# Kernel optimization log

Hardware: AMD Instinct MI355X
Metric: run time of the kernel (lower is better)

## Reference

```python
import jax, jax.numpy as jnp
import numpy as np

B, T, C = 2, 4096, 768
H = 12
HD = C // H  # 64


def setup_inputs() -> dict:
    key = jax.random.key(0)
    k1, k2, k3 = jax.random.split(key, 3)
    scale = 0.02
    x = jax.random.normal(k1, (B, T, C), dtype=jnp.float32)
    w_attn = jax.random.normal(k2, (C, 3 * C), dtype=jnp.float32) * scale
    b_attn = jnp.zeros((3 * C,), dtype=jnp.float32)
    w_proj = jax.random.normal(k3, (C, C), dtype=jnp.float32) * scale
    b_proj = jnp.zeros((C,), dtype=jnp.float32)
    return {"x": x, "w_attn": w_attn, "b_attn": b_attn,
            "w_proj": w_proj, "b_proj": b_proj}


def reference(x, w_attn, b_attn, w_proj, b_proj):
    b, t, c = x.shape
    # QKV projection: (B,T,3C)
    qkv = x @ w_attn + b_attn
    q, k, v = jnp.split(qkv, 3, axis=2)
    # (B,H,T,HD)
    q = q.reshape(b, t, H, HD).transpose(0, 2, 1, 3)
    k = k.reshape(b, t, H, HD).transpose(0, 2, 1, 3)
    v = v.reshape(b, t, H, HD).transpose(0, 2, 1, 3)
    # scores: (B,H,T,T)
    scores = jnp.einsum('bhqd,bhkd->bhqk', q, k) / jnp.sqrt(jnp.float32(HD))
    causal = jnp.tril(jnp.ones((t, t), dtype=bool))
    scores = jnp.where(causal[None, None, :, :], scores, -jnp.inf)
    att = jax.nn.softmax(scores, axis=-1)
    # attn_dropout p=0 -> identity
    y = jnp.einsum('bhqk,bhkd->bhqd', att, v)
    y = y.transpose(0, 2, 1, 3).reshape(b, t, c)
    # output projection (resid_dropout p=0 -> identity)
    return y @ w_proj + b_proj
```

## Files before the change

### kernel.cpp

```cpp
#include <hip/hip_runtime.h>


typedef unsigned short u16;
typedef unsigned int u32;
using bf16x8 = __attribute__((ext_vector_type(8))) short;
using f32x4  = __attribute__((ext_vector_type(4))) float;

__device__ __forceinline__ float bf2f(u16 u) {
  return __uint_as_float(((u32)u) << 16);
}
__device__ __forceinline__ u16 f2bf(float f) {
  u32 u = __float_as_uint(f);
  u += 0x7fffu + ((u >> 16) & 1u);
  return (u16)(u >> 16);
}
__device__ __forceinline__ u32 cvtpk(float lo, float hi) {
  u32 r;
  asm("v_cvt_pk_bf16_f32 %0, %1, %2" : "=v"(r) : "v"(lo), "v"(hi));
  return r;
}

__global__ void fill_sentinel_f32(float* __restrict__ out, int n, float v) {
  const int i0 = blockIdx.x * blockDim.x + threadIdx.x;
  const int stride = gridDim.x * blockDim.x;
  for (int i = i0; i < n; i += stride) out[i] = v;
}

__global__ void convert_f32_bf16(const float* __restrict__ src, u16* __restrict__ dst,
                                 int n) {
  const int i0 = blockIdx.x * blockDim.x + threadIdx.x;
  const int stride = gridDim.x * blockDim.x;
  for (int i = i0; i < n; i += stride) dst[i] = f2bf(src[i]);
}

__global__ void transpose_f32_bf16(const float* __restrict__ in, u16* __restrict__ out,
                                   int R, int C) {
  __shared__ u16 tile[32][33];
  const int c0 = blockIdx.x * 32, r0 = blockIdx.y * 32;
  const int tx = threadIdx.x & 31, ty = threadIdx.x >> 5;
#pragma unroll
  for (int i = 0; i < 32; i += 8)
    tile[ty + i][tx] = f2bf(in[(size_t)(r0 + ty + i) * C + c0 + tx]);
  __syncthreads();
#pragma unroll
  for (int i = 0; i < 32; i += 8)
    out[(size_t)(c0 + ty + i) * R + r0 + tx] = tile[tx][ty + i];
}

#define LDT 72
#define QSCALE 0.18033688011112f

__device__ __forceinline__ void stage_tile(u16* lds, const u16* g, int ld, int tid) {
#pragma unroll
  for (int i = 0; i < 4; ++i) {
    const int idx = i * 256 + tid;
    const int r = idx >> 3, c = (idx & 7) * 8;
    *(uint4*)&lds[r * LDT + c] = *(const uint4*)&g[(size_t)r * ld + c];
  }
}

template <int MODE>
__global__ __launch_bounds__(256, 2)
void gemm128(const u16* __restrict__ A, const u16* __restrict__ Bt,
             const u16* __restrict__ bias, void* __restrict__ O0v,
             u16* __restrict__ O1, u16* __restrict__ O2, int Kd) {
  __shared__ __align__(16) u16 As[128 * LDT];
  __shared__ __align__(16) u16 Bs[128 * LDT];
  const int tid = threadIdx.x;
  const int lane = tid & 63, wave = tid >> 6;
  const int wm = wave >> 1, wn = wave & 1;
  const int l16 = lane & 15, quad = lane >> 4;

  const u16* Ag = A + (size_t)blockIdx.x * 128 * Kd;
  const u16* Bg = Bt + (size_t)blockIdx.y * 128 * Kd;

  f32x4 acc[4][4] = {};
  for (int kt = 0; kt < Kd; kt += 64) {
    stage_tile(As, Ag + kt, Kd, tid);
    stage_tile(Bs, Bg + kt, Kd, tid);
    __syncthreads();
#pragma unroll
    for (int s = 0; s < 2; ++s) {
      bf16x8 af[4], bfr[4];
#pragma unroll
      for (int i = 0; i < 4; ++i) {
        const int m = wm * 64 + i * 16 + l16;
        af[i] = *(const bf16x8*)&As[m * LDT + (s * 4 + quad) * 8];
        const int n = wn * 64 + i * 16 + l16;
        bfr[i] = *(const bf16x8*)&Bs[n * LDT + (s * 4 + quad) * 8];
      }
#pragma unroll
      for (int i = 0; i < 4; ++i)
#pragma unroll
        for (int j = 0; j < 4; ++j)
          acc[i][j] = __builtin_amdgcn_mfma_f32_16x16x32_bf16(af[i], bfr[j],
                                                              acc[i][j], 0, 0, 0);
    }
    __syncthreads();
  }

#pragma unroll
  for (int i = 0; i < 4; ++i) {
    const int mbase = blockIdx.x * 128 + wm * 64 + i * 16 + quad * 4;
#pragma unroll
    for (int j = 0; j < 4; ++j) {
      const int n = blockIdx.y * 128 + wn * 64 + j * 16 + l16;
      const float bv = bf2f(bias[n]);
#pragma unroll
      for (int r = 0; r < 4; ++r) {
        const int m = mbase + r;
        float ov = acc[i][j][r] + bv;
        if (MODE == 0) {
          const int b = m >> 12, t = m & 4095;
          const int which = n / 768;
          const int c = n - which * 768;
          const int h = c >> 6, d = c & 63;
          const size_t bh = (size_t)b * 12 + h;
          if (which == 0) {
            ((u16*)O0v)[((bh * 4096 + t) << 6) + d] = f2bf(ov * QSCALE);
          } else if (which == 1) {
            O1[((bh * 4096 + t) << 6) + d] = f2bf(ov);
          } else {
            O2[((bh << 6) + d) * 4096 + t] = f2bf(ov);
          }
        } else {
          ((float*)O0v)[(size_t)m * 768 + n] = ov;
        }
      }
    }
  }
}

__global__ __launch_bounds__(256, 4)
void attn_chunk(const u16* __restrict__ Q, const u16* __restrict__ K,
                const u16* __restrict__ Vt, u16* __restrict__ Y,
                u16* __restrict__ part_o, float* __restrict__ part_l) {
  const int idx = blockIdx.x;
  const int bh = idx % 24;
  const int cid = 79 - (idx / 24);
  int qt = 0, base = 0, nc = 1;
  for (int q = 0; q < 32; ++q) {
    const int c = (q >> 3) + 1;
    if (cid < base + c) { qt = q; nc = c; break; }
    base += c;
  }
  const int j = cid - base;
  const int Nt = 2 * qt + 2;
  const int kbeg = j * 16;
  const int kend = (kbeg + 16 < Nt) ? kbeg + 16 : Nt;
  const int q0 = qt * 128;
  const int b = bh / 12, h = bh % 12;
  const size_t ho = (size_t)bh * 4096 * 64;
  const u16* Qg = Q + ho + (size_t)q0 * 64;
  const u16* Kg = K + ho;
  const u16* Vg = Vt + ho;

  __shared__ __align__(16) u16 Ks[64 * LDT];
  __shared__ __align__(16) u16 Vs[64 * LDT];

  const int tid = threadIdx.x;
  const int lane = tid & 63, wave = tid >> 6;
  const int l16 = lane & 15, quad = lane >> 4;

  bf16x8 qf[2][2];
#pragma unroll
  for (int rt = 0; rt < 2; ++rt)
#pragma unroll
    for (int s = 0; s < 2; ++s)
      qf[rt][s] = *(const bf16x8*)&Qg[(wave * 32 + rt * 16 + l16) * 64 + s * 32 + quad * 8];

  float lsum[2] = {};
  f32x4 o[2][4] = {};

  for (int kt2 = kbeg; kt2 < kend; ++kt2) {
    const int t0 = kt2 * 64;
    __syncthreads();
    {
      int c = tid;
      *(uint4*)&Ks[(c >> 3) * LDT + (c & 7) * 8] =
          *(const uint4*)&Kg[(size_t)(t0 + (c >> 3)) * 64 + (c & 7) * 8];
      c = tid + 256;
      *(uint4*)&Ks[(c >> 3) * LDT + (c & 7) * 8] =
          *(const uint4*)&Kg[(size_t)(t0 + (c >> 3)) * 64 + (c & 7) * 8];
      c = tid;
      *(uint4*)&Vs[(c >> 3) * LDT + (c & 7) * 8] =
          *(const uint4*)&Vg[(size_t)(c >> 3) * 4096 + t0 + (c & 7) * 8];
      c = tid + 256;
      *(uint4*)&Vs[(c >> 3) * LDT + (c & 7) * 8] =
          *(const uint4*)&Vg[(size_t)(c >> 3) * 4096 + t0 + (c & 7) * 8];
    }
    __syncthreads();

    f32x4 sc[4][2] = {};
#pragma unroll
    for (int s = 0; s < 2; ++s) {
      bf16x8 kf[4];
#pragma unroll
      for (int nt = 0; nt < 4; ++nt)
        kf[nt] = *(const bf16x8*)&Ks[(nt * 16 + l16) * LDT + s * 32 + quad * 8];
#pragma unroll
      for (int nt = 0; nt < 4; ++nt)
#pragma unroll
        for (int rt = 0; rt < 2; ++rt)
          sc[nt][rt] = __builtin_amdgcn_mfma_f32_16x16x32_bf16(kf[nt], qf[rt][s],
                                                               sc[nt][rt], 0, 0, 0);
    }

    u32 pw[4][2][2];
#pragma unroll
    for (int rt = 0; rt < 2; ++rt) {
      const int rowb = q0 + wave * 32 + rt * 16;
      if (t0 + 63 <= rowb) {
#pragma unroll
        for (int nt = 0; nt < 4; ++nt) {
          f32x4 p;
#pragma unroll
          for (int r = 0; r < 4; ++r) {
            p[r] = __builtin_amdgcn_exp2f(sc[nt][rt][r]);
            lsum[rt] += p[r];
          }
          pw[nt][rt][0] = cvtpk(p[0], p[1]);
          pw[nt][rt][1] = cvtpk(p[2], p[3]);
        }
      } else {
        const int qrow = rowb + l16;
#pragma unroll
        for (int nt = 0; nt < 4; ++nt) {
          f32x4 p;
#pragma unroll
          for (int r = 0; r < 4; ++r) {
            float pv = __builtin_amdgcn_exp2f(sc[nt][rt][r]);
            if (t0 + nt * 16 + quad * 4 + r > qrow) pv = 0.f;
            p[r] = pv;
            lsum[rt] += pv;
          }
          pw[nt][rt][0] = cvtpk(p[0], p[1]);
          pw[nt][rt][1] = cvtpk(p[2], p[3]);
        }
      }
    }

#pragma unroll
    for (int s2 = 0; s2 < 2; ++s2) {
      bf16x8 vf[4];
#pragma unroll
      for (int dt = 0; dt < 4; ++dt) {
        const u16* vp = &Vs[(dt * 16 + l16) * LDT + s2 * 32 + quad * 4];
        union { uint2 h[2]; bf16x8 v; } uv;
        uv.h[0] = *(const uint2*)vp;
        uv.h[1] = *(const uint2*)(vp + 16);
        vf[dt] = uv.v;
      }
#pragma unroll
      for (int rt = 0; rt < 2; ++rt) {
        union { u32 w[4]; bf16x8 v; } up;
        up.w[0] = pw[2 * s2][rt][0];
        up.w[1] = pw[2 * s2][rt][1];
        up.w[2] = pw[2 * s2 + 1][rt][0];
        up.w[3] = pw[2 * s2 + 1][rt][1];
#pragma unroll
        for (int dt = 0; dt < 4; ++dt)
          o[rt][dt] = __builtin_amdgcn_mfma_f32_16x16x32_bf16(up.v, vf[dt],
                                                              o[rt][dt], 0, 0, 0);
      }
    }
  }

  float red[2];
#pragma unroll
  for (int rt = 0; rt < 2; ++rt) {
    float rs = lsum[rt];
    rs += __shfl_xor(rs, 16);
    rs += __shfl_xor(rs, 32);
    red[rt] = rs;
  }

  if (nc == 1) {
#pragma unroll
    for (int rt = 0; rt < 2; ++rt)
#pragma unroll
      for (int r = 0; r < 4; ++r) {
        const float inv = 1.f / __shfl(red[rt], quad * 4 + r);
        const int t = q0 + wave * 32 + rt * 16 + quad * 4 + r;
#pragma unroll
        for (int dt = 0; dt < 4; ++dt)
          Y[((size_t)b * 4096 + t) * 768 + h * 64 + dt * 16 + l16] =
              f2bf(o[rt][dt][r] * inv);
      }
  } else {
    const int pslot = bh * 72 + (cid - 8);
    u16* po = part_o + (size_t)pslot * 8192;
    float* pl = part_l + pslot * 128;
#pragma unroll
    for (int rt = 0; rt < 2; ++rt)
#pragma unroll
      for (int r = 0; r < 4; ++r) {
        const float rs = __shfl(red[rt], quad * 4 + r);
        const int row = wave * 32 + rt * 16 + quad * 4 + r;
#pragma unroll
        for (int dt = 0; dt < 4; ++dt)
          po[row * 64 + dt * 16 + l16] = f2bf(o[rt][dt][r]);
        if (l16 == 0) pl[row] = rs;
      }
  }
}

__global__ __launch_bounds__(256, 8)
void attn_combine(const u16* __restrict__ part_o, const float* __restrict__ part_l,
                  u16* __restrict__ Y) {
  const int bh = blockIdx.x, qt = 8 + blockIdx.y;
  const int g = qt >> 3, i = qt & 7;
  const int nc = g + 1;
  const int base = 4 * g * (g + 1) + i * (g + 1);
  const int slot0 = bh * 72 + base - 8;
  const int b = bh / 12, h = bh % 12;
  const int q0 = qt * 128;
  for (int e = threadIdx.x; e < 8192; e += 256) {
    const int row = e >> 6, d = e & 63;
    float Os = 0.f, ls = 0.f;
    for (int c = 0; c < nc; ++c) {
      Os += bf2f(part_o[(size_t)(slot0 + c) * 8192 + e]);
      ls += part_l[(slot0 + c) * 128 + row];
    }
    Y[((size_t)b * 4096 + q0 + row) * 768 + h * 64 + d] = f2bf(Os / ls);
  }
}

extern "C" void kernel_launch(void* const* d_in, const int* in_sizes, int n_in,
                              void* d_out, int out_size, void* d_ws, size_t ws_size,
                              hipStream_t stream) {
  (void)in_sizes; (void)n_in;
  const float* x      = (const float*)d_in[0];
  const float* w_attn = (const float*)d_in[1];
  const float* b_attn = (const float*)d_in[2];
  const float* w_proj = (const float*)d_in[3];
  const float* b_proj = (const float*)d_in[4];
  float* out = (float*)d_out;

  char* ws = (char*)d_ws;
  size_t off = 0;
  auto alloc = [&](size_t bytes) -> void* {
    void* p = ws + off;
    off += (bytes + 255) & ~(size_t)255;
    return p;
  };
  u16* xb  = (u16*)alloc((size_t)8192 * 768 * 2);
  u16* WtA = (u16*)alloc((size_t)2304 * 768 * 2);
  u16* WtP = (u16*)alloc((size_t)768 * 768 * 2);
  u16* ba  = (u16*)alloc(2304 * 2);
  u16* bp  = (u16*)alloc(768 * 2);
  u16* Q   = (u16*)alloc((size_t)6291456 * 2);
  u16* Kp  = (u16*)alloc((size_t)6291456 * 2);
  u16* Vt  = (u16*)alloc((size_t)6291456 * 2);
  u16* Y   = (u16*)alloc((size_t)6291456 * 2);
  u16* part_o  = (u16*)alloc((size_t)24 * 72 * 8192 * 2);
  float* part_l = (float*)alloc((size_t)24 * 72 * 128 * 4);

  if (ws_size < off) {
    fill_sentinel_f32<<<256, 256, 0, stream>>>(out, out_size,
                                               100.0f + (float)(ws_size >> 20));
    return;
  }

  convert_f32_bf16<<<2048, 256, 0, stream>>>(x, xb, 8192 * 768);
  convert_f32_bf16<<<16, 256, 0, stream>>>(b_attn, ba, 2304);
  convert_f32_bf16<<<8, 256, 0, stream>>>(b_proj, bp, 768);
  transpose_f32_bf16<<<dim3(72, 24), 256, 0, stream>>>(w_attn, WtA, 768, 2304);
  transpose_f32_bf16<<<dim3(24, 24), 256, 0, stream>>>(w_proj, WtP, 768, 768);

  gemm128<0><<<dim3(64, 18), 256, 0, stream>>>(xb, WtA, ba, Q, Kp, Vt, 768);
  attn_chunk<<<1920, 256, 0, stream>>>(Q, Kp, Vt, Y, part_o, part_l);
  attn_combine<<<dim3(24, 24), 256, 0, stream>>>(part_o, part_l, Y);
  gemm128<1><<<dim3(64, 6), 256, 0, stream>>>(Y, WtP, bp, out, nullptr, nullptr, 768);
}
```

Baseline: 285.5 us.

## Double-buffer K/V tiles, compute row sums via MFMA, vectorize QKV epilogue stores

The attention chunk kernel now double-buffers its K/V shared-memory tiles. Global loads for the next tile are issued into registers before the current tile's compute and committed afterwards, so each iteration needs one barrier instead of two. Softmax row sums are now taken with an extra MFMA against a ones vector rather than scalar adds and cross-lane shuffles; this sums the bf16-rounded probabilities, which slightly changes the normalization. The QKV GEMM epilogue hoists the index math out of the per-row loop and writes the transposed V output as packed 4-element stores. Together these double LDS use and add register pressure, which may lower occupancy.

```diff
diff --git a/kernel.cpp b/kernel.cpp
--- a/kernel.cpp
+++ b/kernel.cpp
@@ -104,28 +104,36 @@
     const int mbase = blockIdx.x * 128 + wm * 64 + i * 16 + quad * 4;
 #pragma unroll
     for (int j = 0; j < 4; ++j) {
-      const int n = blockIdx.y * 128 + wn * 64 + j * 16 + l16;
+      const int nb = blockIdx.y * 128 + wn * 64 + j * 16;
+      const int n = nb + l16;
       const float bv = bf2f(bias[n]);
-#pragma unroll
-      for (int r = 0; r < 4; ++r) {
-        const int m = mbase + r;
-        float ov = acc[i][j][r] + bv;
-        if (MODE == 0) {
-          const int b = m >> 12, t = m & 4095;
-          const int which = n / 768;
-          const int c = n - which * 768;
-          const int h = c >> 6, d = c & 63;
-          const size_t bh = (size_t)b * 12 + h;
-          if (which == 0) {
-            ((u16*)O0v)[((bh * 4096 + t) << 6) + d] = f2bf(ov * QSCALE);
-          } else if (which == 1) {
-            O1[((bh * 4096 + t) << 6) + d] = f2bf(ov);
-          } else {
-            O2[((bh << 6) + d) * 4096 + t] = f2bf(ov);
-          }
+      if (MODE == 0) {
+        const int which = nb / 768;
+        const int b = mbase >> 12, t = mbase & 4095;
+        const int c = n - which * 768;
+        const int h = c >> 6, d = c & 63;
+        const size_t bh = (size_t)b * 12 + h;
+        if (which == 0) {
+#pragma unroll
+          for (int r = 0; r < 4; ++r)
+            ((u16*)O0v)[((bh * 4096 + t + r) << 6) + d] =
+                f2bf((acc[i][j][r] + bv) * QSCALE);
+        } else if (which == 1) {
+#pragma unroll
+          for (int r = 0; r < 4; ++r)
+            O1[((bh * 4096 + t + r) << 6) + d] = f2bf(acc[i][j][r] + bv);
         } else {
-          ((float*)O0v)[(size_t)m * 768 + n] = ov;
+          ushort4 pk;
+          pk.x = f2bf(acc[i][j][0] + bv);
+          pk.y = f2bf(acc[i][j][1] + bv);
+          pk.z = f2bf(acc[i][j][2] + bv);
+          pk.w = f2bf(acc[i][j][3] + bv);
+          *(ushort4*)&O2[((bh << 6) + (size_t)d) * 4096 + t] = pk;
         }
+      } else {
+#pragma unroll
+        for (int r = 0; r < 4; ++r)
+          ((float*)O0v)[(size_t)(mbase + r) * 768 + n] = acc[i][j][r] + bv;
       }
     }
   }
@@ -155,13 +163,20 @@
   const u16* Kg = K + ho;
   const u16* Vg = Vt + ho;
 
-  __shared__ __align__(16) u16 Ks[64 * LDT];
-  __shared__ __align__(16) u16 Vs[64 * LDT];
+  __shared__ __align__(16) u16 Ks[2][64 * LDT];
+  __shared__ __align__(16) u16 Vs[2][64 * LDT];
 
   const int tid = threadIdx.x;
   const int lane = tid & 63, wave = tid >> 6;
   const int l16 = lane & 15, quad = lane >> 4;
 
+  const int r8 = tid >> 3, c8 = (tid & 7) * 8;
+  const u16* kg0 = Kg + (size_t)r8 * 64 + c8;
+  const u16* kg1 = Kg + (size_t)(r8 + 32) * 64 + c8;
+  const u16* vg0 = Vg + (size_t)r8 * 4096 + c8;
+  const u16* vg1 = Vg + (size_t)(r8 + 32) * 4096 + c8;
+  const int lw0 = r8 * LDT + c8, lw1 = (r8 + 32) * LDT + c8;
+
   bf16x8 qf[2][2];
 #pragma unroll
   for (int rt = 0; rt < 2; ++rt)
@@ -169,27 +184,36 @@
     for (int s = 0; s < 2; ++s)
       qf[rt][s] = *(const bf16x8*)&Qg[(wave * 32 + rt * 16 + l16) * 64 + s * 32 + quad * 8];
 
-  float lsum[2] = {};
+  bf16x8 ones;
+#pragma unroll
+  for (int e = 0; e < 8; ++e) ones[e] = (short)0x3F80;
+
+  f32x4 lacc[2] = {};
   f32x4 o[2][4] = {};
+
+  uint4 kr0, kr1, vr0, vr1;
+  auto issue = [&](int kt2) {
+    kr0 = *(const uint4*)(kg0 + (size_t)kt2 * 4096);
+    kr1 = *(const uint4*)(kg1 + (size_t)kt2 * 4096);
+    vr0 = *(const uint4*)(vg0 + (size_t)kt2 * 64);
+    vr1 = *(const uint4*)(vg1 + (size_t)kt2 * 64);
+  };
+  auto commit = [&](int bf) {
+    *(uint4*)&Ks[bf][lw0] = kr0;
+    *(uint4*)&Ks[bf][lw1] = kr1;
+    *(uint4*)&Vs[bf][lw0] = vr0;
+    *(uint4*)&Vs[bf][lw1] = vr1;
+  };
+
+  issue(kbeg);
+  commit(0);
+  __syncthreads();
+  int cur = 0;
 
   for (int kt2 = kbeg; kt2 < kend; ++kt2) {
     const int t0 = kt2 * 64;
-    __syncthreads();
-    {
-      int c = tid;
-      *(uint4*)&Ks[(c >> 3) * LDT + (c & 7) * 8] =
-          *(const uint4*)&Kg[(size_t)(t0 + (c >> 3)) * 64 + (c & 7) * 8];
-      c = tid + 256;
-      *(uint4*)&Ks[(c >> 3) * LDT + (c & 7) * 8] =
-          *(const uint4*)&Kg[(size_t)(t0 + (c >> 3)) * 64 + (c & 7) * 8];
-      c = tid;
-      *(uint4*)&Vs[(c >> 3) * LDT + (c & 7) * 8] =
-          *(const uint4*)&Vg[(size_t)(c >> 3) * 4096 + t0 + (c & 7) * 8];
-      c = tid + 256;
-      *(uint4*)&Vs[(c >> 3) * LDT + (c & 7) * 8] =
-          *(const uint4*)&Vg[(size_t)(c >> 3) * 4096 + t0 + (c & 7) * 8];
-    }
-    __syncthreads();
+    const bool more = (kt2 + 1 < kend);
+    if (more) issue(kt2 + 1);
 
     f32x4 sc[4][2] = {};
 #pragma unroll
@@ -197,7 +221,7 @@
       bf16x8 kf[4];
 #pragma unroll
       for (int nt = 0; nt < 4; ++nt)
-        kf[nt] = *(const bf16x8*)&Ks[(nt * 16 + l16) * LDT + s * 32 + quad * 8];
+        kf[nt] = *(const bf16x8*)&Ks[cur][(nt * 16 + l16) * LDT + s * 32 + quad * 8];
 #pragma unroll
       for (int nt = 0; nt < 4; ++nt)
 #pragma unroll
@@ -215,10 +239,8 @@
         for (int nt = 0; nt < 4; ++nt) {
           f32x4 p;
 #pragma unroll
-          for (int r = 0; r < 4; ++r) {
+          for (int r = 0; r < 4; ++r)
             p[r] = __builtin_amdgcn_exp2f(sc[nt][rt][r]);
-            lsum[rt] += p[r];
-          }
           pw[nt][rt][0] = cvtpk(p[0], p[1]);
           pw[nt][rt][1] = cvtpk(p[2], p[3]);
         }
@@ -232,7 +254,6 @@
             float pv = __builtin_amdgcn_exp2f(sc[nt][rt][r]);
             if (t0 + nt * 16 + quad * 4 + r > qrow) pv = 0.f;
             p[r] = pv;
-            lsum[rt] += pv;
           }
           pw[nt][rt][0] = cvtpk(p[0], p[1]);
           pw[nt][rt][1] = cvtpk(p[2], p[3]);
@@ -245,10 +266,10 @@
       bf16x8 vf[4];
 #pragma unroll
       for (int dt = 0; dt < 4; ++dt) {
-        const u16* vp = &Vs[(dt * 16 + l16) * LDT + s2 * 32 + quad * 4];
-        union { uint2 h[2]; bf16x8 v; } uv;
-        uv.h[0] = *(const uint2*)vp;
-        uv.h[1] = *(const uint2*)(vp + 16);
+        const u16* vp = &Vs[cur][(dt * 16 + l16) * LDT + s2 * 32 + quad * 4];
+        union { uint2 hv[2]; bf16x8 v; } uv;
+        uv.hv[0] = *(const uint2*)vp;
+        uv.hv[1] = *(const uint2*)(vp + 16);
         vf[dt] = uv.v;
       }
 #pragma unroll
@@ -262,17 +283,16 @@
         for (int dt = 0; dt < 4; ++dt)
           o[rt][dt] = __builtin_amdgcn_mfma_f32_16x16x32_bf16(up.v, vf[dt],
                                                               o[rt][dt], 0, 0, 0);
-      }
-    }
-  }
-
-  float red[2];
-#pragma unroll
-  for (int rt = 0; rt < 2; ++rt) {
-    float rs = lsum[rt];
-    rs += __shfl_xor(rs, 16);
-    rs += __shfl_xor(rs, 32);
-    red[rt] = rs;
+        lacc[rt] = __builtin_amdgcn_mfma_f32_16x16x32_bf16(up.v, ones,
+                                                           lacc[rt], 0, 0, 0);
+      }
+    }
+
+    if (more) {
+      commit(cur ^ 1);
+      __syncthreads();
+      cur ^= 1;
+    }
   }
 
   if (nc == 1) {
@@ -280,7 +300,7 @@
     for (int rt = 0; rt < 2; ++rt)
 #pragma unroll
       for (int r = 0; r < 4; ++r) {
-        const float inv = 1.f / __shfl(red[rt], quad * 4 + r);
+        const float inv = 1.f / lacc[rt][r];
         const int t = q0 + wave * 32 + rt * 16 + quad * 4 + r;
 #pragma unroll
         for (int dt = 0; dt < 4; ++dt)
@@ -295,12 +315,11 @@
     for (int rt = 0; rt < 2; ++rt)
 #pragma unroll
       for (int r = 0; r < 4; ++r) {
-        const float rs = __shfl(red[rt], quad * 4 + r);
         const int row = wave * 32 + rt * 16 + quad * 4 + r;
 #pragma unroll
         for (int dt = 0; dt < 4; ++dt)
           po[row * 64 + dt * 16 + l16] = f2bf(o[rt][dt][r]);
-        if (l16 == 0) pl[row] = rs;
+        if (l16 == 0) pl[row] = lacc[rt][r];
       }
   }
 }
```

After: 350.0 us. 1.23x slower.
